# Optimization experiments

Hardware: AMD Instinct MI355X
Metric: run time of the kernel (lower is better)

## Reference

```python
import jax, jax.numpy as jnp
import numpy as np

N_EMBD = 1024
N_HEAD = 16
HEAD_DIM = N_EMBD // N_HEAD
B, T = 2, 2048


def setup_inputs() -> dict:
    key = jax.random.key(0)
    ks = jax.random.split(key, 12)
    s = 0.02
    inp = {
        "x": jax.random.normal(ks[0], (B, T, N_EMBD), dtype=jnp.float32),
        "ln1_g": jnp.ones((N_EMBD,), jnp.float32),
        "ln1_b": jnp.zeros((N_EMBD,), jnp.float32),
        "ln2_g": jnp.ones((N_EMBD,), jnp.float32),
        "ln2_b": jnp.zeros((N_EMBD,), jnp.float32),
        "W_qkv": jax.random.normal(ks[1], (N_EMBD, 3 * N_EMBD), jnp.float32) * s,
        "b_qkv": jnp.zeros((3 * N_EMBD,), jnp.float32),
        "W_o": jax.random.normal(ks[2], (N_EMBD, N_EMBD), jnp.float32) * s,
        "b_o": jnp.zeros((N_EMBD,), jnp.float32),
        "W_fc": jax.random.normal(ks[3], (N_EMBD, 4 * N_EMBD), jnp.float32) * s,
        "b_fc": jnp.zeros((4 * N_EMBD,), jnp.float32),
        "W_proj": jax.random.normal(ks[4], (4 * N_EMBD, N_EMBD), jnp.float32) * s,
        "b_proj": jnp.zeros((N_EMBD,), jnp.float32),
    }
    return inp


def _layernorm(x, g, b, eps=1e-5):
    mu = jnp.mean(x, axis=-1, keepdims=True)
    var = jnp.var(x, axis=-1, keepdims=True)
    return (x - mu) * jax.lax.rsqrt(var + eps) * g + b


def _block(x, ln1_g, ln1_b, ln2_g, ln2_b, W_qkv, b_qkv, W_o, b_o, W_fc, b_fc, W_proj, b_proj):
    # --- attention sub-block (pre-LN) ---
    h = _layernorm(x, ln1_g, ln1_b)
    qkv = h @ W_qkv + b_qkv                     # [B,T,3E]
    q, k, v = jnp.split(qkv, 3, axis=-1)
    def split_heads(t):
        return t.reshape(B, T, N_HEAD, HEAD_DIM).transpose(0, 2, 1, 3)  # [B,H,T,D]
    q, k, v = split_heads(q), split_heads(k), split_heads(v)
    scores = jnp.einsum("bhqd,bhkd->bhqk", q, k) / (HEAD_DIM ** 0.5)
    causal = jnp.tril(jnp.ones((T, T), dtype=bool))
    scores = jnp.where(causal, scores, jnp.float32(-jnp.inf))
    probs = jax.nn.softmax(scores, axis=-1)
    attn = jnp.einsum("bhqk,bhkd->bhqd", probs, v)        # [B,H,T,D]
    attn = attn.transpose(0, 2, 1, 3).reshape(B, T, N_EMBD)
    x = x + attn @ W_o + b_o
    # --- MLP sub-block (pre-LN) ---
    h = _layernorm(x, ln2_g, ln2_b)
    h = jax.nn.gelu(h @ W_fc + b_fc, approximate=False)
    x = x + h @ W_proj + b_proj
    return x


def reference(x, ln1_g, ln1_b, ln2_g, ln2_b, W_qkv, b_qkv, W_o, b_o, W_fc, b_fc, W_proj, b_proj):
    return _block(x, ln1_g, ln1_b, ln2_g, ln2_b, W_qkv, b_qkv, W_o, b_o, W_fc, b_fc, W_proj, b_proj)
```

## Files before the change

kernel.cpp:

```cpp
#include <hip/hip_runtime.h>
#include <hip/hip_bf16.h>


#define TT 2048
#define EE 1024
#define NH 16
#define HD 64

#define AS1 __attribute__((address_space(1)))
#define AS3 __attribute__((address_space(3)))

using bf16x8 = __bf16 __attribute__((ext_vector_type(8)));
using bf16x4 = __bf16 __attribute__((ext_vector_type(4)));
using f32x4  = float __attribute__((ext_vector_type(4)));

template<int N> __device__ __forceinline__ void vm_wait() {
    if constexpr (N == 0)      asm volatile("s_waitcnt vmcnt(0)" ::: "memory");
    else if constexpr (N == 2) asm volatile("s_waitcnt vmcnt(2)" ::: "memory");
    else if constexpr (N == 3) asm volatile("s_waitcnt vmcnt(3)" ::: "memory");
    else if constexpr (N == 4) asm volatile("s_waitcnt vmcnt(4)" ::: "memory");
    else if constexpr (N == 6) asm volatile("s_waitcnt vmcnt(6)" ::: "memory");
    else                       asm volatile("s_waitcnt vmcnt(8)" ::: "memory");
}

__device__ __forceinline__ float gelu_fast(float v) {
    float z  = v * 0.70710678118f;
    float az = fabsf(z);
    float t  = __builtin_amdgcn_rcpf(__builtin_fmaf(0.3275911f, az, 1.0f));
    float p  = t * __builtin_fmaf(t,
                   __builtin_fmaf(t,
                     __builtin_fmaf(t,
                       __builtin_fmaf(t, 1.061405429f, -1.453152027f),
                       1.421413741f),
                     -0.284496736f),
                   0.254829592f);
    float e  = __expf(-az * az);
    float er = copysignf(1.0f - p * e, z);
    return 0.5f * v * (1.0f + er);
}

__global__ __launch_bounds__(256) void convt_kernel(const float* __restrict__ W,
                                                    __bf16* __restrict__ WT,
                                                    int K, int N) {
    __shared__ __bf16 t[32][33];
    int n0 = blockIdx.x * 32, k0 = blockIdx.y * 32;
    int tid = threadIdx.x;
    int r = tid >> 3, c4 = (tid & 7) * 4;
    float4 v = *(const float4*)(W + (size_t)(k0 + r) * N + n0 + c4);
    t[r][c4 + 0] = (__bf16)v.x; t[r][c4 + 1] = (__bf16)v.y;
    t[r][c4 + 2] = (__bf16)v.z; t[r][c4 + 3] = (__bf16)v.w;
    __syncthreads();
    bf16x4 o;
    o[0] = t[c4 + 0][r]; o[1] = t[c4 + 1][r];
    o[2] = t[c4 + 2][r]; o[3] = t[c4 + 3][r];
    *(bf16x4*)(WT + (size_t)(n0 + r) * K + k0 + c4) = o;
}

__global__ __launch_bounds__(256) void ln_kernel(const float* __restrict__ x,
                                                 const float* __restrict__ g,
                                                 const float* __restrict__ bta,
                                                 __bf16* __restrict__ out) {
    int row = blockIdx.x;
    int tid = threadIdx.x;
    const float4 xv = *(const float4*)(x + (size_t)row * EE + tid * 4);
    float s  = xv.x + xv.y + xv.z + xv.w;
    float ss = xv.x*xv.x + xv.y*xv.y + xv.z*xv.z + xv.w*xv.w;
    __shared__ float rs[256], rss[256];
    rs[tid] = s; rss[tid] = ss;
    __syncthreads();
    for (int st = 128; st > 0; st >>= 1) {
        if (tid < st) { rs[tid] += rs[tid+st]; rss[tid] += rss[tid+st]; }
        __syncthreads();
    }
    float mean = rs[0] * (1.0f / EE);
    float var  = rss[0] * (1.0f / EE) - mean * mean;
    float rstd = rsqrtf(var + 1e-5f);
    const float4 gv = *(const float4*)(g + tid * 4);
    const float4 bv = *(const float4*)(bta + tid * 4);
    bf16x4 ov;
    ov[0] = (__bf16)((xv.x - mean) * rstd * gv.x + bv.x);
    ov[1] = (__bf16)((xv.y - mean) * rstd * gv.y + bv.y);
    ov[2] = (__bf16)((xv.z - mean) * rstd * gv.z + bv.z);
    ov[3] = (__bf16)((xv.w - mean) * rstd * gv.w + bv.w);
    *(bf16x4*)(out + (size_t)row * EE + tid * 4) = ov;
}

template<int TM, int TN, bool GELU, bool RESID, bool QKV, typename CT>
__global__ __launch_bounds__(256) void gemm_bt_kernel(const __bf16* __restrict__ A,
                                                      const __bf16* __restrict__ BT,
                                                      const float* __restrict__ bias,
                                                      const float* resid, CT* C,
                                                      __bf16* vT,
                                                      int M, int N, int K) {
    constexpr int MT = TM / 32;
    constexpr int NT = TN / 32;
    constexpr int LOADS = TM / 64 + TN / 64;
    constexpr int NBUF  = (LOADS <= 3) ? 4 : 3;
    constexpr int DEPTH = NBUF - 1;
    constexpr int WAITN = (DEPTH - 1) * LOADS;
    __shared__ __align__(16) __bf16 As[NBUF][TM][32];
    __shared__ __align__(16) __bf16 Bs[NBUF][TN][32];
    int tid = threadIdx.x, wave = tid >> 6, lane = tid & 63;
    int quad = lane >> 4, l16 = lane & 15;
    int wm = wave >> 1, wn = wave & 1;
    int m0 = blockIdx.y * TM, n0 = blockIdx.x * TN;

    f32x4 acc[MT][NT] = {};

    int srow = wave * 16 + (lane >> 2);
    int scol = (((lane & 3) ^ ((lane >> 3) & 3)) * 8);
    int xcol = ((quad ^ ((l16 >> 1) & 3)) * 8);

    auto STAGE = [&](int buf, int kt) {
        int kb = kt << 5;
#pragma unroll
        for (int p = 0; p < TM / 64; p++) {
            const __bf16* g = A + (size_t)(m0 + p * 64 + srow) * K + kb + scol;
            __builtin_amdgcn_global_load_lds((AS1 const void*)g,
                                             (AS3 void*)&As[buf][p * 64 + wave * 16][0],
                                             16, 0, 0);
        }
#pragma unroll
        for (int p = 0; p < TN / 64; p++) {
            const __bf16* g = BT + (size_t)(n0 + p * 64 + srow) * K + kb + scol;
            __builtin_amdgcn_global_load_lds((AS1 const void*)g,
                                             (AS3 void*)&Bs[buf][p * 64 + wave * 16][0],
                                             16, 0, 0);
        }
    };

    auto COMPUTE = [&](int cur) {
        bf16x8 af[MT], bfr[NT];
#pragma unroll
        for (int mt = 0; mt < MT; mt++)
            af[mt] = *(const bf16x8*)(&As[cur][wm * (MT * 16) + mt * 16 + l16][xcol]);
#pragma unroll
        for (int nt = 0; nt < NT; nt++)
            bfr[nt] = *(const bf16x8*)(&Bs[cur][wn * (NT * 16) + nt * 16 + l16][xcol]);
#pragma unroll
        for (int mt = 0; mt < MT; mt++)
#pragma unroll
            for (int nt = 0; nt < NT; nt++)
                acc[mt][nt] = __builtin_amdgcn_mfma_f32_16x16x32_bf16(af[mt], bfr[nt],
                                                                      acc[mt][nt], 0, 0, 0);
    };

    const int nk = K >> 5;
#pragma unroll
    for (int i = 0; i < DEPTH; ++i) STAGE(i, i);
    vm_wait<WAITN>();
    __builtin_amdgcn_s_barrier();

    int t = 0;
    for (; t + DEPTH < nk; ++t) {
        STAGE((t + DEPTH) % NBUF, t + DEPTH);
        COMPUTE(t % NBUF);
        vm_wait<WAITN>();
        __builtin_amdgcn_s_barrier();
    }
    for (; t < nk; ++t) {
        COMPUTE(t % NBUF);
        if (t + 1 < nk) {
            int rem = nk - 2 - t;
            if (rem >= 1) vm_wait<LOADS>();
            else          vm_wait<0>();
            __builtin_amdgcn_s_barrier();
        }
    }

#pragma unroll
    for (int nt = 0; nt < NT; nt++) {
        int c = n0 + wn * (NT * 16) + nt * 16 + l16;
        float bv = bias[c];
#pragma unroll
        for (int mt = 0; mt < MT; mt++) {
#pragma unroll
            for (int r = 0; r < 4; r++) {
                int row = m0 + wm * (MT * 16) + mt * 16 + quad * 4 + r;
                float v = acc[mt][nt][r] + bv;
                if (GELU)  v = gelu_fast(v);
                if (RESID) v += resid[(size_t)row * N + c];
                if (!QKV) {
                    C[(size_t)row * N + c] = (CT)v;
                } else {
                    if (c < 2 * EE) {
                        ((__bf16*)C)[(size_t)row * (2 * EE) + c] = (__bf16)v;
                    } else {
                        int cv = c - 2 * EE;
                        int bb = row >> 11, tt = row & (TT - 1);
                        vT[((size_t)(bb * NH + (cv >> 6)) * HD + (cv & 63)) * TT + tt] =
                            (__bf16)v;
                    }
                }
            }
        }
    }
}

__global__ __launch_bounds__(256) void flash_attn_kernel(const __bf16* __restrict__ qkv,
                                                         const __bf16* __restrict__ vT,
                                                         __bf16* __restrict__ out) {
    int h = blockIdx.y, b = blockIdx.z;
    int tid = threadIdx.x, wave = tid >> 6, lane = tid & 63;
    int quad = lane >> 4, l16 = lane & 15;

    __shared__ __align__(16) __bf16 Ks[128 * 72];
    __shared__ __align__(16) __bf16 Ps[4][16 * 136];

    size_t base = (size_t)b * TT * (2 * EE);

    int srow = tid >> 3;
    int scol = (tid & 7) * 8;
    const __bf16* kbase  = qkv + base + EE + h * HD + scol;
    const __bf16* vrow = vT + (size_t)(b * NH + h) * HD * TT + (size_t)l16 * TT + quad * 8;
    __bf16* Psw = &Ps[wave][0];

    int nTiles = (int)gridDim.x * 2;

    for (int pass = 0; pass < 2; pass++) {
        int qt = pass == 0 ? (nTiles - 1 - blockIdx.x) : blockIdx.x;
        int q0 = qt * 64;

        int qrow = q0 + wave * 16 + l16;
        const __bf16* qp = qkv + base + (size_t)qrow * (2 * EE) + h * HD;
        bf16x8 aq0 = *(const bf16x8*)(qp + quad * 8);
        bf16x8 aq1 = *(const bf16x8*)(qp + 32 + quad * 8);

        f32x4 oacc[4] = {};
        float lsum[4] = {0.f, 0.f, 0.f, 0.f};
        int qg_base = q0 + wave * 16 + quad * 4;

        int nIter = (qt >> 1) + 1;

        bf16x8 kr[4];
#pragma unroll
        for (int p = 0; p < 4; p++)
            kr[p] = *(const bf16x8*)(kbase + (size_t)(32 * p + srow) * (2 * EE));

        for (int kt = 0; kt < nIter; ++kt) {
            int k0 = kt * 128;
#pragma unroll
            for (int p = 0; p < 4; p++)
                *(bf16x8*)(&Ks[(32 * p + srow) * 72 + scol]) = kr[p];
            __syncthreads();

            bf16x8 vf[4][4];
#pragma unroll
            for (int dt = 0; dt < 4; dt++)
#pragma unroll
                for (int w = 0; w < 4; w++)
                    vf[dt][w] = *(const bf16x8*)(vrow + (size_t)dt * (16 * TT) + k0 + w * 32);

            if (kt < nIter - 1) {
                int kn = k0 + 128;
#pragma unroll
                for (int p = 0; p < 4; p++)
                    kr[p] = *(const bf16x8*)(kbase + (size_t)(kn + 32 * p + srow) * (2 * EE));
            }

            f32x4 s[8];
#pragma unroll
            for (int nt = 0; nt < 8; nt++) {
                bf16x8 bk0 = *(const bf16x8*)(&Ks[(nt * 16 + l16) * 72 + quad * 8]);
                bf16x8 bk1 = *(const bf16x8*)(&Ks[(nt * 16 + l16) * 72 + 32 + quad * 8]);
                f32x4 z = {};
                z = __builtin_amdgcn_mfma_f32_16x16x32_bf16(aq0, bk0, z, 0, 0, 0);
                s[nt] = __builtin_amdgcn_mfma_f32_16x16x32_bf16(aq1, bk1, z, 0, 0, 0);
            }

            bool maskt = (kt == nIter - 1);
#pragma unroll
            for (int nt = 0; nt < 8; nt++) {
                int key = k0 + nt * 16 + l16;
                int cb = 2 * nt + (l16 >> 3);
#pragma unroll
                for (int r = 0; r < 4; r++) {
                    float p;
                    if (maskt && key > qg_base + r) p = 0.0f;
                    else p = __expf(fminf(s[nt][r] * 0.125f, 30.0f));
                    lsum[r] += p;
                    int q = quad * 4 + r;
                    int col = (((cb & 8) | ((cb - 2 * q) & 7)) << 3) | (l16 & 7);
                    Psw[q * 136 + col] = (__bf16)p;
                }
            }

#pragma unroll
            for (int w = 0; w < 4; w++) {
                int cbr = 4 * w + quad;
                int colr = ((cbr & 8) | ((cbr - 2 * l16) & 7)) << 3;
                bf16x8 ap = *(const bf16x8*)(&Psw[l16 * 136 + colr]);
#pragma unroll
                for (int dt = 0; dt < 4; dt++)
                    oacc[dt] = __builtin_amdgcn_mfma_f32_16x16x32_bf16(ap, vf[dt][w],
                                                                       oacc[dt], 0, 0, 0);
            }
            __syncthreads();
        }

#pragma unroll
        for (int off = 1; off < 16; off <<= 1)
#pragma unroll
            for (int r = 0; r < 4; r++) lsum[r] += __shfl_xor(lsum[r], off);
#pragma unroll
        for (int dt = 0; dt < 4; dt++) {
#pragma unroll
            for (int r = 0; r < 4; r++) {
                int qg = qg_base + r;
                out[((size_t)b * TT + qg) * EE + h * HD + dt * 16 + l16] =
                    (__bf16)(oacc[dt][r] / lsum[r]);
            }
        }
    }
}

extern "C" void kernel_launch(void* const* d_in, const int* in_sizes, int n_in,
                              void* d_out, int out_size, void* d_ws, size_t ws_size,
                              hipStream_t stream) {
    const float* x     = (const float*)d_in[0];
    const float* ln1g  = (const float*)d_in[1];
    const float* ln1b  = (const float*)d_in[2];
    const float* ln2g  = (const float*)d_in[3];
    const float* ln2b  = (const float*)d_in[4];
    const float* Wqkv  = (const float*)d_in[5];
    const float* bqkv  = (const float*)d_in[6];
    const float* Wo    = (const float*)d_in[7];
    const float* bo    = (const float*)d_in[8];
    const float* Wfc   = (const float*)d_in[9];
    const float* bfc   = (const float*)d_in[10];
    const float* Wproj = (const float*)d_in[11];
    const float* bproj = (const float*)d_in[12];
    float* out = (float*)d_out;

    const int M = 2 * TT;

    __bf16* ws = (__bf16*)d_ws;
    __bf16* regQ   = ws;
    __bf16* regS   = ws + 16777216;
    __bf16* WfcT   = ws + 20971520;
    __bf16* qkv    = regQ;
    __bf16* vT     = regQ + 8388608;
    __bf16* WqkvT  = regQ + 12582912;
    __bf16* WoT    = regQ + 15728640;
    __bf16* ff     = regQ;
    __bf16* h1 = regS, *atn = regS, *h2 = regS;
    __bf16* WprojT = regS;
    float*  x1 = out;

    convt_kernel<<<dim3(3 * EE / 32, EE / 32), 256, 0, stream>>>(Wqkv, WqkvT, EE, 3 * EE);
    convt_kernel<<<dim3(EE / 32, EE / 32), 256, 0, stream>>>(Wo, WoT, EE, EE);
    convt_kernel<<<dim3(4 * EE / 32, EE / 32), 256, 0, stream>>>(Wfc, WfcT, EE, 4 * EE);

    ln_kernel<<<M, 256, 0, stream>>>(x, ln1g, ln1b, h1);
    gemm_bt_kernel<128, 128, false, false, true, __bf16>
        <<<dim3(3 * EE / 128, M / 128), 256, 0, stream>>>(
        h1, WqkvT, bqkv, nullptr, qkv, vT, M, 3 * EE, EE);
    flash_attn_kernel<<<dim3(TT / 128, NH, 2), 256, 0, stream>>>(qkv, vT, atn);
    gemm_bt_kernel<128, 64, false, true, false, float>
        <<<dim3(EE / 64, M / 128), 256, 0, stream>>>(
        atn, WoT, bo, x, x1, nullptr, M, EE, EE);
    ln_kernel<<<M, 256, 0, stream>>>(x1, ln2g, ln2b, h2);
    gemm_bt_kernel<128, 128, true, false, false, __bf16>
        <<<dim3(4 * EE / 128, M / 128), 256, 0, stream>>>(
        h2, WfcT, bfc, nullptr, ff, nullptr, M, 4 * EE, EE);
    convt_kernel<<<dim3(EE / 32, 4 * EE / 32), 256, 0, stream>>>(Wproj, WprojT, 4 * EE, EE);
    gemm_bt_kernel<128, 64, false, true, false, float>
        <<<dim3(EE / 64, M / 128), 256, 0, stream>>>(
        ff, WprojT, bproj, x1, out, nullptr, M, EE, 4 * EE);
}
```

Baseline: 426.9 us.

## Split-K the MLP down-projection with atomics and prefetch V in attention

The final W_proj GEMM (K=4096) now runs as a two-way split-K over a grid z-dimension. Each half atomically adds its partial result into the output buffer, which already holds the residual x1, so the explicit residual read is dropped and bias is added only by the first split. This doubles the block count to raise parallelism, at the cost of float atomic traffic and nondeterministic summation order. In flash attention, the V fragments for the next key tile are loaded into registers after the PV MFMAs instead of at the top of each iteration. The barriers are also swapped for raw s_barrier with explicit lgkmcnt waits, to overlap global V loads with compute.

```diff
diff --git a/kernel.cpp b/kernel.cpp
--- a/kernel.cpp
+++ b/kernel.cpp
@@ -21,6 +21,15 @@
     else if constexpr (N == 4) asm volatile("s_waitcnt vmcnt(4)" ::: "memory");
     else if constexpr (N == 6) asm volatile("s_waitcnt vmcnt(6)" ::: "memory");
     else                       asm volatile("s_waitcnt vmcnt(8)" ::: "memory");
+}
+
+__device__ __forceinline__ void barrier_after_dswrite() {
+    asm volatile("s_waitcnt lgkmcnt(0)" ::: "memory");
+    __builtin_amdgcn_s_barrier();
+}
+__device__ __forceinline__ void barrier_raw() {
+    asm volatile("" ::: "memory");
+    __builtin_amdgcn_s_barrier();
 }
 
 __device__ __forceinline__ float gelu_fast(float v) {
@@ -85,7 +94,7 @@
     *(bf16x4*)(out + (size_t)row * EE + tid * 4) = ov;
 }
 
-template<int TM, int TN, bool GELU, bool RESID, bool QKV, typename CT>
+template<int TM, int TN, bool GELU, bool RESID, bool QKV, bool ATOMIC, typename CT>
 __global__ __launch_bounds__(256) void gemm_bt_kernel(const __bf16* __restrict__ A,
                                                       const __bf16* __restrict__ BT,
                                                       const float* __restrict__ bias,
@@ -95,7 +104,7 @@
     constexpr int MT = TM / 32;
     constexpr int NT = TN / 32;
     constexpr int LOADS = TM / 64 + TN / 64;
-    constexpr int NBUF  = (LOADS <= 3) ? 4 : 3;
+    constexpr int NBUF  = ATOMIC ? 3 : ((LOADS <= 3) ? 4 : 3);
     constexpr int DEPTH = NBUF - 1;
     constexpr int WAITN = (DEPTH - 1) * LOADS;
     __shared__ __align__(16) __bf16 As[NBUF][TM][32];
@@ -105,6 +114,9 @@
     int wm = wave >> 1, wn = wave & 1;
     int m0 = blockIdx.y * TM, n0 = blockIdx.x * TN;
 
+    const int klen = ATOMIC ? (K >> 1) : K;
+    const int koff = ATOMIC ? (int)blockIdx.z * klen : 0;
+
     f32x4 acc[MT][NT] = {};
 
     int srow = wave * 16 + (lane >> 2);
@@ -112,7 +124,7 @@
     int xcol = ((quad ^ ((l16 >> 1) & 3)) * 8);
 
     auto STAGE = [&](int buf, int kt) {
-        int kb = kt << 5;
+        int kb = koff + (kt << 5);
 #pragma unroll
         for (int p = 0; p < TM / 64; p++) {
             const __bf16* g = A + (size_t)(m0 + p * 64 + srow) * K + kb + scol;
@@ -145,7 +157,7 @@
                                                                       acc[mt][nt], 0, 0, 0);
     };
 
-    const int nk = K >> 5;
+    const int nk = klen >> 5;
 #pragma unroll
     for (int i = 0; i < DEPTH; ++i) STAGE(i, i);
     vm_wait<WAITN>();
@@ -171,7 +183,7 @@
 #pragma unroll
     for (int nt = 0; nt < NT; nt++) {
         int c = n0 + wn * (NT * 16) + nt * 16 + l16;
-        float bv = bias[c];
+        float bv = (!ATOMIC || blockIdx.z == 0) ? bias[c] : 0.0f;
 #pragma unroll
         for (int mt = 0; mt < MT; mt++) {
 #pragma unroll
@@ -180,7 +192,9 @@
                 float v = acc[mt][nt][r] + bv;
                 if (GELU)  v = gelu_fast(v);
                 if (RESID) v += resid[(size_t)row * N + c];
-                if (!QKV) {
+                if (ATOMIC) {
+                    atomicAdd((float*)&C[(size_t)row * N + c], v);
+                } else if (!QKV) {
                     C[(size_t)row * N + c] = (CT)v;
                 } else {
                     if (c < 2 * EE) {
@@ -236,20 +250,19 @@
 #pragma unroll
         for (int p = 0; p < 4; p++)
             kr[p] = *(const bf16x8*)(kbase + (size_t)(32 * p + srow) * (2 * EE));
+        bf16x8 vf[4][4];
+#pragma unroll
+        for (int dt = 0; dt < 4; dt++)
+#pragma unroll
+            for (int w = 0; w < 4; w++)
+                vf[dt][w] = *(const bf16x8*)(vrow + (size_t)dt * (16 * TT) + w * 32);
 
         for (int kt = 0; kt < nIter; ++kt) {
             int k0 = kt * 128;
 #pragma unroll
             for (int p = 0; p < 4; p++)
                 *(bf16x8*)(&Ks[(32 * p + srow) * 72 + scol]) = kr[p];
-            __syncthreads();
-
-            bf16x8 vf[4][4];
-#pragma unroll
-            for (int dt = 0; dt < 4; dt++)
-#pragma unroll
-                for (int w = 0; w < 4; w++)
-                    vf[dt][w] = *(const bf16x8*)(vrow + (size_t)dt * (16 * TT) + k0 + w * 32);
+            barrier_after_dswrite();
 
             if (kt < nIter - 1) {
                 int kn = k0 + 128;
@@ -295,7 +308,16 @@
                     oacc[dt] = __builtin_amdgcn_mfma_f32_16x16x32_bf16(ap, vf[dt][w],
                                                                        oacc[dt], 0, 0, 0);
             }
-            __syncthreads();
+
+            if (kt < nIter - 1) {
+                int kn = k0 + 128;
+#pragma unroll
+                for (int dt = 0; dt < 4; dt++)
+#pragma unroll
+                    for (int w = 0; w < 4; w++)
+                        vf[dt][w] = *(const bf16x8*)(vrow + (size_t)dt * (16 * TT) + kn + w * 32);
+            }
+            barrier_raw();
         }
 
 #pragma unroll
@@ -352,19 +374,19 @@
     convt_kernel<<<dim3(4 * EE / 32, EE / 32), 256, 0, stream>>>(Wfc, WfcT, EE, 4 * EE);
 
     ln_kernel<<<M, 256, 0, stream>>>(x, ln1g, ln1b, h1);
-    gemm_bt_kernel<128, 128, false, false, true, __bf16>
+    gemm_bt_kernel<128, 128, false, false, true, false, __bf16>
         <<<dim3(3 * EE / 128, M / 128), 256, 0, stream>>>(
         h1, WqkvT, bqkv, nullptr, qkv, vT, M, 3 * EE, EE);
     flash_attn_kernel<<<dim3(TT / 128, NH, 2), 256, 0, stream>>>(qkv, vT, atn);
-    gemm_bt_kernel<128, 64, false, true, false, float>
+    gemm_bt_kernel<128, 64, false, true, false, false, float>
         <<<dim3(EE / 64, M / 128), 256, 0, stream>>>(
         atn, WoT, bo, x, x1, nullptr, M, EE, EE);
     ln_kernel<<<M, 256, 0, stream>>>(x1, ln2g, ln2b, h2);
-    gemm_bt_kernel<128, 128, true, false, false, __bf16>
+    gemm_bt_kernel<128, 128, true, false, false, false, __bf16>
         <<<dim3(4 * EE / 128, M / 128), 256, 0, stream>>>(
         h2, WfcT, bfc, nullptr, ff, nullptr, M, 4 * EE, EE);
     convt_kernel<<<dim3(EE / 32, 4 * EE / 32), 256, 0, stream>>>(Wproj, WprojT, 4 * EE, EE);
-    gemm_bt_kernel<128, 64, false, true, false, float>
-        <<<dim3(EE / 64, M / 128), 256, 0, stream>>>(
-        ff, WprojT, bproj, x1, out, nullptr, M, EE, 4 * EE);
-}
+    gemm_bt_kernel<128, 64, false, false, false, true, float>
+        <<<dim3(EE / 64, M / 128, 2), 256, 0, stream>>>(
+        ff, WprojT, bproj, nullptr, out, nullptr, M, EE, 4 * EE);
+}
```

Result: slower. 453.8 us (+6.3%).
